# Performance work log

Hardware: AMD Instinct MI355X
Metric: run time of the kernel (lower is better)

The kernel has to match this reference:

```python
import jax, jax.numpy as jnp
import numpy as np

CL1_K = 25
CL2_K = 25


def cheb_stack(L, x0, K):
    # x0: (V, M) -> (K, V, M) Chebyshev basis T_k(L) x0
    if K == 1:
        return x0[None]
    x1 = L @ x0
    if K == 2:
        return jnp.stack([x0, x1])

    def step(carry, _):
        xm1, xm2 = carry
        xk = 2.0 * (L @ xm1) - xm2
        return (xk, xm1), xk

    _, rest = jax.lax.scan(step, (x1, x0), None, length=K - 2)
    return jnp.concatenate([x0[None], x1[None], rest], axis=0)


def graph_conv(x, L, W, b, K):
    # x: (B, C, V) -> (B, Fout, V); matches torch Graph_Conv permute/view logic
    B, C, V = x.shape
    x0 = x.transpose(2, 1, 0).reshape(V, C * B)
    xs = cheb_stack(L, x0, K)                              # (K, V, C*B)
    xs = xs.reshape(K, V, C, B).transpose(3, 1, 2, 0)      # (B, V, C, K)
    xs = xs.reshape(B * V, C * K)
    y = xs @ W.T + b                                       # (B*V, Fout)
    return y.reshape(B, V, -1).transpose(0, 2, 1)


def maxpool4(x):
    B, C, V = x.shape
    return x.reshape(B, C, V // 4, 4).max(axis=-1)


def setup_inputs() -> dict:
    key = jax.random.key(0)
    ks = jax.random.split(key, 10)
    B, C, V, Vp = 32, 16, 4000, 4096
    CL1_F, CL2_F, FC_F = 64, 128, 10
    x = jax.random.normal(ks[0], (B, C, V), dtype=jnp.float32)
    perm = jax.random.permutation(ks[1], Vp)
    # rescaled Laplacians, scaled for stable 25-step recurrence
    L1 = jax.random.normal(ks[2], (Vp, Vp), dtype=jnp.float32) * (0.3 / np.sqrt(Vp))
    L2 = jax.random.normal(ks[3], (Vp // 4, Vp // 4), dtype=jnp.float32) * (0.3 / np.sqrt(Vp // 4))
    W1 = jax.random.normal(ks[4], (CL1_F, C * CL1_K), dtype=jnp.float32) * np.sqrt(2.0 / (C * CL1_K + CL1_F))
    b1 = jnp.zeros((CL1_F,), dtype=jnp.float32)
    W2 = jax.random.normal(ks[5], (CL2_F, CL1_F * CL2_K), dtype=jnp.float32) * np.sqrt(2.0 / (CL1_F * CL2_K + CL2_F))
    b2 = jnp.zeros((CL2_F,), dtype=jnp.float32)
    FC_IN = CL2_F * Vp // 16
    Wfc = jax.random.normal(ks[6], (FC_F, FC_IN), dtype=jnp.float32) * np.sqrt(2.0 / (FC_IN + FC_F))
    bfc = jnp.zeros((FC_F,), dtype=jnp.float32)
    return {"x": x, "perm": perm, "L1": L1, "L2": L2, "W1": W1, "b1": b1,
            "W2": W2, "b2": b2, "Wfc": Wfc, "bfc": bfc}


def reference(x, perm, L1, L2, W1, b1, W2, b2, Wfc, bfc):
    # BatchNorm1d(affine=False), training-mode batch statistics
    mu = x.mean(axis=(0, 2), keepdims=True)
    var = x.var(axis=(0, 2), keepdims=True)
    x = (x - mu) / jnp.sqrt(var + 1e-5)
    # Permute: zero-pad vertices to len(perm), then index
    B, C, V = x.shape
    Vp = perm.shape[0]
    x = jnp.pad(x, ((0, 0), (0, 0), (0, Vp - V)))[:, :, perm]
    x = jax.nn.relu(graph_conv(x, L1, W1, b1, CL1_K))
    x = maxpool4(x)
    x = jax.nn.relu(graph_conv(x, L2, W2, b2, CL2_K))
    x = maxpool4(x)
    x = x.reshape(B, -1)
    # dropout in eval mode (identity)
    return x @ Wfc.T + bfc
```

## Files before the change

kernel.cpp:

```cpp
#include <hip/hip_runtime.h>

typedef _Float16 half8 __attribute__((ext_vector_type(8)));
typedef _Float16 half4 __attribute__((ext_vector_type(4)));
typedef float f32x4 __attribute__((ext_vector_type(4)));

__device__ __forceinline__ void gload_lds16(const void* g, void* l) {
  __builtin_amdgcn_global_load_lds((const __attribute__((address_space(1))) void*)g,
                                   (__attribute__((address_space(3))) void*)l, 16, 0, 0);
}

__global__ __launch_bounds__(256) void k_bn_partial(const float* __restrict__ x,
                                                    float* __restrict__ part) {
  const int c = blockIdx.x & 15;
  const int seg = blockIdx.x >> 4;
  const int t = threadIdx.x;
  float s = 0.f, s2 = 0.f;
  for (int b = 0; b < 32; ++b) {
    const float* row = x + (size_t)(b * 16 + c) * 4000 + seg * 500;
    for (int v = t; v < 500; v += 256) {
      float val = row[v];
      s += val;
      s2 += val * val;
    }
  }
#pragma unroll
  for (int off = 32; off > 0; off >>= 1) {
    s += __shfl_down(s, off);
    s2 += __shfl_down(s2, off);
  }
  __shared__ float rs_[4], rs2_[4];
  if ((t & 63) == 0) { rs_[t >> 6] = s; rs2_[t >> 6] = s2; }
  __syncthreads();
  if (t == 0) {
    part[c * 8 + seg] = rs_[0] + rs_[1] + rs_[2] + rs_[3];
    part[128 + c * 8 + seg] = rs2_[0] + rs2_[1] + rs2_[2] + rs2_[3];
  }
}

__global__ void k_bn_final(const float* __restrict__ part, float* __restrict__ musig) {
  const int c = threadIdx.x;
  if (c < 16) {
    float S = 0.f, S2 = 0.f;
#pragma unroll
    for (int seg = 0; seg < 8; ++seg) {
      S += part[c * 8 + seg];
      S2 += part[128 + c * 8 + seg];
    }
    const float inv = 1.f / 128000.f;
    float mu = S * inv;
    float var = S2 * inv - mu * mu;
    musig[c] = mu;
    musig[16 + c] = rsqrtf(var + 1e-5f);
  }
}

__global__ __launch_bounds__(256) void k_build_x0(const float* __restrict__ x,
                                                  const int* __restrict__ perm,
                                                  const float* __restrict__ musig,
                                                  _Float16* __restrict__ X0) {
  const int idx = blockIdx.x * 256 + threadIdx.x;
  const int v = idx & 4095;
  const int m = idx >> 12;
  const int b = m & 31;
  const int c = m >> 5;
  const int pv = perm[v];
  float val = 0.f;
  if (pv < 4000)
    val = (x[((size_t)(b * 16 + c)) * 4000 + pv] - musig[c]) * musig[16 + c] * 0.0625f;
  X0[idx] = (_Float16)val;
}

__global__ __launch_bounds__(256) void k_cvt_f16(const float* __restrict__ s,
                                                 _Float16* __restrict__ d, int n) {
  const int i = (blockIdx.x * 256 + threadIdx.x) * 4;
  if (i >= n) return;
  f32x4 v = *(const f32x4*)(s + i);
  half4 h;
  h[0] = (_Float16)v[0]; h[1] = (_Float16)v[1];
  h[2] = (_Float16)v[2]; h[3] = (_Float16)v[3];
  *(half4*)(d + i) = h;
}

__global__ __launch_bounds__(256) void k_zero(_Float16* __restrict__ p, int n8) {
  const int i = blockIdx.x * 256 + threadIdx.x;
  if (i < n8) *(half8*)(p + (size_t)i * 8) = half8{};
}

__global__ __launch_bounds__(256) void k_prep_w(const float* __restrict__ W,
                                                _Float16* __restrict__ Wp,
                                                int F, int shiftC, int kround) {
  const int idx = blockIdx.x * 256 + threadIdx.x;
  const int CS = 1 << shiftC;
  const int KPtot = kround * CS;
  if (idx >= F * KPtot) return;
  const int f = idx / KPtot;
  const int rem = idx - f * KPtot;
  const int k = rem >> shiftC;
  const int c = rem & (CS - 1);
  float v = 0.f;
  if (k < 25) v = W[(size_t)f * (CS * 25) + c * 25 + k];
  Wp[idx] = (_Float16)v;
}

__global__ __launch_bounds__(512, 2) void k_cheb8(const _Float16* __restrict__ Xprev,
                                                  const _Float16* __restrict__ Lm,
                                                  _Float16* __restrict__ P,
                                                  int V, int NT, int bxbits, int bybits) {
  __shared__ _Float16 lds[3][24576];
  const int t = threadIdx.x;
  const int lane = t & 63;
  const int ln = lane & 15;
  const int g = lane >> 4;
  const int g16 = g << 4;
  const int w = t >> 6;
  const int wm = w >> 2, wn = w & 3;
  const int bid = blockIdx.x;
  const int bx = bid & ((1 << bxbits) - 1);
  const int by = (bid >> bxbits) & ((1 << bybits) - 1);
  const int kq = bid >> (bxbits + bybits);
  const int v0 = bx * 256, m0 = by * 128;
  const size_t rs = (size_t)V * 2;
  const int koffB = kq * NT * 128;

  const char* Ag = (const char*)Xprev + (size_t)m0 * rs + koffB;
  const char* Bg = (const char*)Lm + (size_t)v0 * rs + koffB;

  f32x4 acc[4][4] = {};

  auto stageHalf = [&](int buf, int tt, int half) {
    char* Lb = (char*)&lds[buf][0];
#pragma unroll
    for (int j = 0; j < 3; ++j) {
      const int idx = half * 1536 + j * 512 + t;
      if (idx < 1024) {
        const int row = idx >> 3, c8 = idx & 7;
        gload_lds16(Ag + (size_t)row * rs + tt * 128 + ((c8 ^ (row & 7)) << 4),
                    Lb + idx * 16);
      } else {
        const int bi = idx - 1024;
        const int row = bi >> 3, c8 = bi & 7;
        gload_lds16(Bg + (size_t)row * rs + tt * 128 + ((c8 ^ (row & 7)) << 4),
                    Lb + 16384 + bi * 16);
      }
    }
  };

  stageHalf(0, 0, 0); stageHalf(0, 0, 1);
  stageHalf(1, 1, 0); stageHalf(1, 1, 1);
  asm volatile("s_waitcnt vmcnt(6)" ::: "memory");
  asm volatile("s_barrier" ::: "memory");

  for (int tt = 0; tt < NT; ++tt) {
    const int cur = tt % 3;
    const int nxt = (tt + 2) % 3;
    const char* A = (const char*)&lds[cur][0];
    const char* B = A + 16384;
#pragma unroll
    for (int kk = 0; kk < 2; ++kk) {
      half8 a[4], b[4];
#pragma unroll
      for (int mi = 0; mi < 4; ++mi) {
        const int ar = wm * 64 + mi * 16 + ln;
        a[mi] = *(const half8*)(A + ar * 128 + ((kk * 64 + g16) ^ ((ar & 7) << 4)));
      }
#pragma unroll
      for (int ni = 0; ni < 4; ++ni) {
        const int br = wn * 64 + ni * 16 + ln;
        b[ni] = *(const half8*)(B + br * 128 + ((kk * 64 + g16) ^ ((br & 7) << 4)));
      }
      if (tt + 2 < NT) stageHalf(nxt, tt + 2, kk);
      if (kk == 1) {
        if (tt + 2 < NT) {
          asm volatile("s_waitcnt vmcnt(6)" ::: "memory");
        } else {
          asm volatile("s_waitcnt vmcnt(0)" ::: "memory");
        }
      }
      asm volatile("s_barrier" ::: "memory");
      asm volatile("s_waitcnt lgkmcnt(0)" ::: "memory");
      __builtin_amdgcn_sched_barrier(0);
      __builtin_amdgcn_s_setprio(1);
#pragma unroll
      for (int mi = 0; mi < 4; ++mi)
#pragma unroll
        for (int ni = 0; ni < 4; ++ni)
          acc[mi][ni] = __builtin_amdgcn_mfma_f32_16x16x32_f16(a[mi], b[ni], acc[mi][ni], 0, 0, 0);
      __builtin_amdgcn_s_setprio(0);
      asm volatile("s_barrier" ::: "memory");
    }
  }

  _Float16* Pq = P + (size_t)kq * 2097152;
#pragma unroll
  for (int mi = 0; mi < 4; ++mi) {
#pragma unroll
    for (int ni = 0; ni < 4; ++ni) {
      const int vv = v0 + wn * 64 + ni * 16 + ln;
      const int mmb = m0 + wm * 64 + mi * 16 + g * 4;
#pragma unroll
      for (int r = 0; r < 4; ++r)
        Pq[(size_t)(mmb + r) * V + vv] = (_Float16)acc[mi][ni][r];
    }
  }
}

__global__ __launch_bounds__(256) void k_cheb_red4(const _Float16* __restrict__ P,
                                                   const _Float16* __restrict__ Xm2,
                                                   _Float16* __restrict__ Xout,
                                                   float alpha, float beta) {
  const size_t i = ((size_t)blockIdx.x * 256 + threadIdx.x) * 8;
  float s[8] = {};
#pragma unroll
  for (int p = 0; p < 4; ++p) {
    half8 v = *(const half8*)(P + (size_t)p * 2097152 + i);
#pragma unroll
    for (int j = 0; j < 8; ++j) s[j] += (float)v[j];
  }
  half8 xm2 = {};
  if (beta != 0.f) xm2 = *(const half8*)(Xm2 + i);
  half8 o;
#pragma unroll
  for (int j = 0; j < 8; ++j) o[j] = (_Float16)(alpha * s[j] - beta * (float)xm2[j]);
  *(half8*)(Xout + i) = o;
}

template <int FT>
__global__ __launch_bounds__(256, 2) void k_dense(const _Float16* __restrict__ Wp,
                                                  const _Float16* __restrict__ XS,
                                                  const float* __restrict__ bias,
                                                  float* __restrict__ Yt,
                                                  int Vv, int shiftC, int nsteps,
                                                  int Ntot, float ascale, float bscale) {
  __shared__ _Float16 Alds[2][FT * 64];
  __shared__ _Float16 Blds[2][64 * 64];
  const int t = threadIdx.x;
  const int lane = t & 63;
  const int g = lane >> 4;
  const int w = t >> 6;
  const int n0 = blockIdx.x * 64;
  const int b = n0 / Vv;
  const int vb = n0 % Vv;
  const int Kp = nsteps * 64;
  const int cmask = (1 << shiftC) - 1;
  const size_t plane = 2097152;

  f32x4 acc[FT / 16] = {};

  auto stage = [&](int buf, int s) {
    const int q0 = s * 64;
    char* A = (char*)&Alds[buf][0];
    char* B = (char*)&Blds[buf][0];
#pragma unroll
    for (int j = 0; j < FT / 32; ++j) {
      const int ch = j * 256 + t;
      const int f = ch >> 3, c8 = ch & 7;
      gload_lds16((const char*)Wp + ((size_t)f * Kp + q0) * 2 + ((c8 ^ (f & 7)) << 4),
                  A + ch * 16);
    }
#pragma unroll
    for (int j = 0; j < 2; ++j) {
      const int ch = j * 256 + t;
      const int q = ch >> 3, c8 = ch & 7;
      const int qq = q0 + q;
      const int k = qq >> shiftC, c = qq & cmask;
      const int sz = (q >> 3) & 7;
      gload_lds16((const char*)XS + ((size_t)k * plane + (size_t)(c * 32 + b) * Vv + vb) * 2 +
                      ((c8 ^ sz) << 4),
                  B + ch * 16);
    }
  };

  stage(0, 0);

  for (int s = 0; s < nsteps; ++s) {
    const int cur = s & 1;
    if (s + 1 < nsteps) {
      stage(cur ^ 1, s + 1);
      if constexpr (FT == 64) {
        asm volatile("s_waitcnt vmcnt(4)" ::: "memory");
      } else {
        asm volatile("s_waitcnt vmcnt(6)" ::: "memory");
      }
    } else {
      asm volatile("s_waitcnt vmcnt(0)" ::: "memory");
    }
    asm volatile("s_barrier" ::: "memory");
    const _Float16* A = &Alds[cur][0];
    const _Float16* B = &Blds[cur][0];
#pragma unroll
    for (int kk = 0; kk < 2; ++kk) {
      half8 bf;
      const int c = lane & 15;
#pragma unroll
      for (int j = 0; j < 8; ++j) {
        const int q = kk * 32 + g * 8 + j;
        const int sz = (q >> 3) & 7;
        bf[j] = B[q * 64 + ((w * 16 + c) ^ (sz << 3))];
      }
#pragma unroll
      for (int mi = 0; mi < FT / 16; ++mi) {
        const int ar = mi * 16 + c;
        half8 af = *(const half8*)((const char*)A + ar * 128 +
                                   ((kk * 64 + g * 16) ^ ((ar & 7) << 4)));
        acc[mi] = __builtin_amdgcn_mfma_f32_16x16x32_f16(af, bf, acc[mi], 0, 0, 0);
      }
    }
    asm volatile("s_barrier" ::: "memory");
  }

  const int n = n0 + w * 16 + (lane & 15);
#pragma unroll
  for (int mi = 0; mi < FT / 16; ++mi) {
#pragma unroll
    for (int r = 0; r < 4; ++r) {
      const int f = mi * 16 + g * 4 + r;
      Yt[(size_t)f * Ntot + n] = fmaxf(ascale * acc[mi][r] + bscale * bias[f], 0.f);
    }
  }
}

__global__ __launch_bounds__(256) void k_pool1(const float* __restrict__ Yt,
                                               _Float16* __restrict__ X2) {
  const int idx = blockIdx.x * 256 + threadIdx.x;
  const int v2 = idx & 1023;
  const int rest = idx >> 10;
  const int b = rest & 31;
  const int f = rest >> 5;
  f32x4 q = *(const f32x4*)(Yt + (size_t)f * 131072 + b * 4096 + v2 * 4);
  float mx = fmaxf(fmaxf(q[0], q[1]), fmaxf(q[2], q[3]));
  X2[(size_t)(f * 32 + b) * 1024 + v2] = (_Float16)(mx * 0.015625f);
}

__global__ __launch_bounds__(256) void k_pool2(const float* __restrict__ Yt,
                                               float* __restrict__ p2) {
  const int idx = blockIdx.x * 256 + threadIdx.x;
  const int v3 = idx & 255;
  const int rest = idx >> 8;
  const int f = rest & 127;
  const int b = rest >> 7;
  f32x4 q = *(const f32x4*)(Yt + (size_t)f * 32768 + b * 1024 + v3 * 4);
  float mx = fmaxf(fmaxf(q[0], q[1]), fmaxf(q[2], q[3]));
  p2[(size_t)b * 32768 + f * 256 + v3] = mx;
}

__global__ __launch_bounds__(256) void k_fc_part(const float* __restrict__ p2,
                                                 const float* __restrict__ Wfc,
                                                 float* __restrict__ partF) {
  const int b = blockIdx.x >> 3;
  const int seg = blockIdx.x & 7;
  const int t = threadIdx.x;
  const int lane = t & 63;
  const int w = t >> 6;
  const int base = seg * 4096;
  float acc[10];
#pragma unroll
  for (int o = 0; o < 10; ++o) acc[o] = 0.f;
  const float* pb = p2 + (size_t)b * 32768 + base;
  for (int i = t; i < 4096; i += 256) {
    float p = pb[i];
#pragma unroll
    for (int o = 0; o < 10; ++o) acc[o] += p * Wfc[(size_t)o * 32768 + base + i];
  }
#pragma unroll
  for (int off = 32; off > 0; off >>= 1)
#pragma unroll
    for (int o = 0; o < 10; ++o) acc[o] += __shfl_down(acc[o], off);
  __shared__ float rws[10][4];
  if (lane == 0) {
#pragma unroll
    for (int o = 0; o < 10; ++o) rws[o][w] = acc[o];
  }
  __syncthreads();
  if (t < 10) partF[blockIdx.x * 10 + t] =
      rws[t][0] + rws[t][1] + rws[t][2] + rws[t][3];
}

__global__ void k_fc_final(const float* __restrict__ partF,
                           const float* __restrict__ bfc,
                           float* __restrict__ out) {
  const int t = threadIdx.x;
  if (t < 320) {
    const int b = t / 10, o = t - b * 10;
    float s = 0.f;
#pragma unroll
    for (int seg = 0; seg < 8; ++seg) s += partF[(b * 8 + seg) * 10 + o];
    out[b * 10 + o] = 64.f * s + bfc[o];
  }
}

extern "C" void kernel_launch(void* const* d_in, const int* in_sizes, int n_in,
                              void* d_out, int out_size, void* d_ws, size_t ws_size,
                              hipStream_t stream) {
  (void)in_sizes; (void)n_in; (void)out_size; (void)ws_size;
  const float* x = (const float*)d_in[0];
  const int* perm = (const int*)d_in[1];
  const float* L1 = (const float*)d_in[2];
  const float* L2 = (const float*)d_in[3];
  const float* W1 = (const float*)d_in[4];
  const float* b1 = (const float*)d_in[5];
  const float* W2 = (const float*)d_in[6];
  const float* b2 = (const float*)d_in[7];
  const float* Wfc = (const float*)d_in[8];
  const float* bfc = (const float*)d_in[9];
  float* out = (float*)d_out;

  char* ws = (char*)d_ws;
  size_t off = 0;
  auto alloc = [&](size_t bytes) {
    char* p = ws + off;
    off += (bytes + 255) & ~(size_t)255;
    return p;
  };
  _Float16* L1h = (_Float16*)alloc(16777216ull * 2);
  _Float16* L2h = (_Float16*)alloc(1048576ull * 2);
  _Float16* W1p = (_Float16*)alloc(64ull * 448 * 2);
  _Float16* W2p = (_Float16*)alloc(128ull * 1664 * 2);
  float* part = (float*)alloc(256 * 4);
  float* musig = (float*)alloc(32 * 4);
  float* partF = (float*)alloc(2560 * 4);
  _Float16* XS = (_Float16*)alloc(28ull * 2097152 * 2);
  float* Yt = (float*)alloc(64ull * 131072 * 4);
  float* p2 = (float*)alloc(32ull * 128 * 256 * 4);
  _Float16* Pq = (_Float16*)Yt;

  const size_t plane = 2097152;

  k_cvt_f16<<<16384, 256, 0, stream>>>(L1, L1h, 16777216);
  k_cvt_f16<<<1024, 256, 0, stream>>>(L2, L2h, 1048576);
  k_prep_w<<<112, 256, 0, stream>>>(W1, W1p, 64, 4, 28);
  k_prep_w<<<832, 256, 0, stream>>>(W2, W2p, 128, 6, 26);
  k_zero<<<3072, 256, 0, stream>>>(XS + 25 * plane, 786432);
  k_bn_partial<<<128, 256, 0, stream>>>(x, part);
  k_bn_final<<<1, 64, 0, stream>>>(part, musig);
  k_build_x0<<<8192, 256, 0, stream>>>(x, perm, musig, XS);

  for (int k = 1; k < 25; ++k) {
    k_cheb8<<<256, 512, 0, stream>>>(XS + (size_t)(k - 1) * plane, L1h, Pq, 4096, 16, 4, 2);
    k_cheb_red4<<<1024, 256, 0, stream>>>(
        Pq, XS + (size_t)(k >= 2 ? k - 2 : 0) * plane, XS + (size_t)k * plane,
        (k == 1) ? 1.f : 2.f, (k == 1) ? 0.f : 1.f);
  }
  k_dense<64><<<dim3(2048, 1), 256, 0, stream>>>(W1p, XS, b1, Yt, 4096, 4, 7,
                                                 131072, 16.f, 1.f);
  k_pool1<<<8192, 256, 0, stream>>>(Yt, XS);
  for (int k = 1; k < 25; ++k) {
    k_cheb8<<<256, 512, 0, stream>>>(XS + (size_t)(k - 1) * plane, L2h, Pq, 1024, 4, 2, 4);
    k_cheb_red4<<<1024, 256, 0, stream>>>(
        Pq, XS + (size_t)(k >= 2 ? k - 2 : 0) * plane, XS + (size_t)k * plane,
        (k == 1) ? 1.f : 2.f, (k == 1) ? 0.f : 1.f);
  }
  k_dense<128><<<dim3(512, 1), 256, 0, stream>>>(W2p, XS, b2, Yt, 1024, 6, 26,
                                                 32768, 1.f, 0.015625f);
  k_pool2<<<4096, 256, 0, stream>>>(Yt, p2);
  k_fc_part<<<256, 256, 0, stream>>>(p2, Wfc, partF);
  k_fc_final<<<1, 320, 0, stream>>>(partF, bfc, out);
}
```

Measured before the change: 1.248 ms.

## Replace split-K cheb8 plus reduction with fused single-pass kernel for layer 2

For the second graph-conv layer (V=1024), the split-K k_cheb8 GEMM and the separate k_cheb_red4 reduction are replaced by k_cheb2. This new kernel computes 64x64 tiles over the full K=1024 with a three-stage LDS pipeline and applies the Chebyshev recurrence (alpha*LX - beta*Xm2) directly in its epilogue. That removes the partial-product round trip through global memory and one launch per step. The launch bound of k_cheb8 also changes from 2 to 1 blocks per CU, which may let it use more registers but lowers occupancy. The epilogue writes are scalar and strided, so stores are less coalesced.

```diff
diff --git a/kernel.cpp b/kernel.cpp
--- a/kernel.cpp
+++ b/kernel.cpp
@@ -102,7 +102,7 @@
   Wp[idx] = (_Float16)v;
 }
 
-__global__ __launch_bounds__(512, 2) void k_cheb8(const _Float16* __restrict__ Xprev,
+__global__ __launch_bounds__(512, 1) void k_cheb8(const _Float16* __restrict__ Xprev,
                                                   const _Float16* __restrict__ Lm,
                                                   _Float16* __restrict__ P,
                                                   int V, int NT, int bxbits, int bybits) {
@@ -222,6 +222,105 @@
 #pragma unroll
   for (int j = 0; j < 8; ++j) o[j] = (_Float16)(alpha * s[j] - beta * (float)xm2[j]);
   *(half8*)(Xout + i) = o;
+}
+
+__global__ __launch_bounds__(256, 2) void k_cheb2(const _Float16* __restrict__ Xprev,
+                                                  const _Float16* __restrict__ Lm,
+                                                  const _Float16* __restrict__ Xm2,
+                                                  _Float16* __restrict__ Xout,
+                                                  float alpha, float beta) {
+  __shared__ _Float16 lds[3][8192];
+  const int t = threadIdx.x;
+  const int lane = t & 63;
+  const int ln = lane & 15;
+  const int g = lane >> 4;
+  const int g16 = g << 4;
+  const int w = t >> 6;
+  const int wm = w >> 1, wn = w & 1;
+  const int bx = blockIdx.x & 15;
+  const int by = blockIdx.x >> 4;
+  const int v0 = bx * 64, m0 = by * 64;
+  const size_t rs = 2048;
+
+  const char* Ag = (const char*)Xprev + (size_t)m0 * rs;
+  const char* Bg = (const char*)Lm + (size_t)v0 * rs;
+
+  f32x4 acc[2][2] = {};
+
+  auto stageHalf = [&](int buf, int tt, int half) {
+    const char* src = (half == 0) ? Ag : Bg;
+    char* dst0 = (char*)&lds[buf][0] + half * 8192;
+#pragma unroll
+    for (int j = 0; j < 2; ++j) {
+      const int idx = j * 256 + t;
+      const int row = idx >> 3, c8 = idx & 7;
+      gload_lds16(src + (size_t)row * rs + tt * 128 + ((c8 ^ (row & 7)) << 4),
+                  dst0 + idx * 16);
+    }
+  };
+
+  stageHalf(0, 0, 0); stageHalf(0, 0, 1);
+  stageHalf(1, 1, 0); stageHalf(1, 1, 1);
+  asm volatile("s_waitcnt vmcnt(4)" ::: "memory");
+  asm volatile("s_barrier" ::: "memory");
+
+  for (int tt = 0; tt < 16; ++tt) {
+    const int cur = tt % 3;
+    const int nxt = (tt + 2) % 3;
+    const char* A = (const char*)&lds[cur][0];
+    const char* B = A + 8192;
+    half8 a[2][2], b[2][2];
+#pragma unroll
+    for (int kk = 0; kk < 2; ++kk) {
+#pragma unroll
+      for (int mi = 0; mi < 2; ++mi) {
+        const int ar = wm * 32 + mi * 16 + ln;
+        a[kk][mi] = *(const half8*)(A + ar * 128 + ((kk * 64 + g16) ^ ((ar & 7) << 4)));
+      }
+#pragma unroll
+      for (int ni = 0; ni < 2; ++ni) {
+        const int br = wn * 32 + ni * 16 + ln;
+        b[kk][ni] = *(const half8*)(B + br * 128 + ((kk * 64 + g16) ^ ((br & 7) << 4)));
+      }
+    }
+    if (tt + 2 < 16) {
+      stageHalf(nxt, tt + 2, 0);
+      stageHalf(nxt, tt + 2, 1);
+      asm volatile("s_waitcnt vmcnt(4)" ::: "memory");
+    } else {
+      asm volatile("s_waitcnt vmcnt(0)" ::: "memory");
+    }
+    asm volatile("s_barrier" ::: "memory");
+    asm volatile("s_waitcnt lgkmcnt(0)" ::: "memory");
+    __builtin_amdgcn_sched_barrier(0);
+    __builtin_amdgcn_s_setprio(1);
+#pragma unroll
+    for (int kk = 0; kk < 2; ++kk)
+#pragma unroll
+      for (int mi = 0; mi < 2; ++mi)
+#pragma unroll
+        for (int ni = 0; ni < 2; ++ni)
+          acc[mi][ni] = __builtin_amdgcn_mfma_f32_16x16x32_f16(a[kk][mi], b[kk][ni],
+                                                               acc[mi][ni], 0, 0, 0);
+    __builtin_amdgcn_s_setprio(0);
+    asm volatile("s_barrier" ::: "memory");
+  }
+
+#pragma unroll
+  for (int mi = 0; mi < 2; ++mi) {
+#pragma unroll
+    for (int ni = 0; ni < 2; ++ni) {
+      const int vv = v0 + wn * 32 + ni * 16 + ln;
+      const int mmb = m0 + wm * 32 + mi * 16 + g * 4;
+#pragma unroll
+      for (int r = 0; r < 4; ++r) {
+        const size_t idx = (size_t)(mmb + r) * 1024 + vv;
+        float val = alpha * acc[mi][ni][r];
+        if (beta != 0.f) val -= (float)Xm2[idx];
+        Xout[idx] = (_Float16)val;
+      }
+    }
+  }
 }
 
 template <int FT>
@@ -444,9 +543,9 @@
                                                  131072, 16.f, 1.f);
   k_pool1<<<8192, 256, 0, stream>>>(Yt, XS);
   for (int k = 1; k < 25; ++k) {
-    k_cheb8<<<256, 512, 0, stream>>>(XS + (size_t)(k - 1) * plane, L2h, Pq, 1024, 4, 2, 4);
-    k_cheb_red4<<<1024, 256, 0, stream>>>(
-        Pq, XS + (size_t)(k >= 2 ? k - 2 : 0) * plane, XS + (size_t)k * plane,
+    k_cheb2<<<512, 256, 0, stream>>>(
+        XS + (size_t)(k - 1) * plane, L2h,
+        XS + (size_t)(k >= 2 ? k - 2 : 0) * plane, XS + (size_t)k * plane,
         (k == 1) ? 1.f : 2.f, (k == 1) ? 0.f : 1.f);
   }
   k_dense<128><<<dim3(512, 1), 256, 0, stream>>>(W2p, XS, b2, Yt, 1024, 6, 26,
```

Measured after the change: 1.147 ms. -8.1%, faster.
